# Performance work log

Hardware: AMD Instinct MI355X
Metric: run time of the kernel (lower is better)

The kernel has to match this reference:

```python
import jax, jax.numpy as jnp
import numpy as np
from jax import lax

N, P, Z, L = 1000, 50000, 10, 5


def setup_inputs() -> dict:
    key = jax.random.key(0)
    ks = jax.random.split(key, 9)
    data = jax.random.normal(ks[0], (N, P), dtype=jnp.float32)
    mean_z = jax.random.normal(ks[1], (N, Z), dtype=jnp.float32)
    A = jax.random.normal(ks[2], (Z, Z), dtype=jnp.float32) * 0.1
    var_z = A @ A.T + 0.01 * jnp.eye(Z, dtype=jnp.float32)  # PSD
    mean_w = jax.random.normal(ks[3], (L, Z, P), dtype=jnp.float32) * 0.01
    var_w = jax.random.uniform(ks[4], (L, Z), dtype=jnp.float32) + 0.1   # positive
    alpha = jax.nn.softmax(jax.random.normal(ks[5], (L, Z, P), dtype=jnp.float32), axis=-1)
    tau_0 = jax.random.uniform(ks[6], (L, Z), dtype=jnp.float32) + 0.5   # positive prior precision
    pi = jax.nn.softmax(jax.random.normal(ks[7], (Z, P), dtype=jnp.float32), axis=-1)
    tau = jnp.array(1.0, dtype=jnp.float32)
    return dict(data=data, mean_z=mean_z, var_z=var_z, mean_w=mean_w,
                var_w=var_w, alpha=alpha, tau_0=tau_0, pi=pi, tau=tau)


def _log_bf(z, s2, s0):
    s0_inv = 1.0 / s0
    s2ps0inv = s2 + s0_inv
    return 0.5 * (jnp.log(s2) - jnp.log(s2ps0inv) + z ** 2 * (s0_inv / s2ps0inv))


def reference(data, mean_z, var_z, mean_w, var_w, alpha, tau_0, pi, tau):
    n_dim = data.shape[0]
    l_dim, z_dim, p_dim = mean_w.shape

    # FactorModel.moments
    mean_zz = mean_z.T @ mean_z + n_dim * var_z            # [z, z]
    # LoadingModel.moments (only mean_w moment is needed)
    W0 = jnp.sum(mean_w * alpha, axis=0)                    # [z, p]

    def factor_body(kdx, carry):
        W, mw, vw, al = carry
        not_k = jnp.where(jnp.arange(z_dim) != kdx, size=z_dim - 1)[0]  # [z-1]
        E_zpzk = mean_zz[kdx][not_k]                        # [z-1]
        E_zzk = mean_zz[kdx, kdx]                           # scalar
        Wk = W[kdx]                                         # [p]
        Wnk = W[not_k]                                      # [z-1, p]
        RtZk = mean_z[:, kdx] @ data - Wnk.T @ E_zpzk       # [p]

        def effect_body(ldx, ecarry):
            Wk, mw, vw, al = ecarry
            Wkl = Wk - mw[ldx, kdx] * al[ldx, kdx]          # [p] residualized
            E_RtZk = RtZk - E_zzk * Wkl                     # [p]
            u_var = jnp.reciprocal(tau * E_zzk + tau_0[ldx, kdx])  # scalar
            u_mean = tau * u_var * E_RtZk                   # [p]
            Z_s = E_RtZk / E_zzk * jnp.sqrt(E_zzk * tau)    # [p]
            s2_s = 1.0 / (E_zzk * tau)
            log_bf = _log_bf(Z_s, s2_s, tau_0[ldx, kdx])
            alpha_kl = jax.nn.softmax(jnp.log(pi[kdx]) + log_bf)   # [p]
            Wk_new = Wkl + u_mean * alpha_kl
            return (Wk_new,
                    mw.at[ldx, kdx].set(u_mean),
                    vw.at[ldx, kdx].set(u_var),
                    al.at[ldx, kdx].set(alpha_kl))

        Wk, mw, vw, al = lax.fori_loop(0, l_dim, effect_body, (Wk, mw, vw, al))
        return (W.at[kdx].set(Wk), mw, vw, al)

    W, mw, vw, al = lax.fori_loop(0, z_dim, factor_body, (W0, mean_w, var_w, alpha))
    return mw, vw, al
```

## Files before the change

### kernel.cpp

```cpp
#include <hip/hip_runtime.h>
#include <math.h>

#define N_DIM 1000
#define P_DIM 50000
#define Z_DIM 10
#define L_DIM 5
#define NSTEP 50

#define NTP 256
#define NBP 196
#define NSPLIT 4
#define NCHUNK 250

#define NT1 256
#define PPT 4
#define PBLK (NT1 * PPT)
#define NBLK 49
#define NEG_BIG (-3.0e38f)
#define SPIN_MAX 32768

constexpr size_t ZP       = (size_t)Z_DIM * P_DIM;
constexpr size_t OFF_ZTR  = 0;
constexpr size_t OFF_PART = ZP;
constexpr size_t PART_F   = (size_t)NSTEP * 64 * 2;
constexpr size_t OFF_W    = ZP + PART_F;
constexpr size_t OFF_ZZ   = OFF_W + ZP;
constexpr size_t WS_ZERO_BYTES = (ZP + PART_F) * sizeof(float);

constexpr size_t OUT_MW = 0;
constexpr size_t OUT_VW = (size_t)L_DIM * Z_DIM * P_DIM;
constexpr size_t OUT_AL = OUT_VW + (size_t)L_DIM * Z_DIM;

__device__ inline void online_merge(float& m, float& e, float m2, float e2) {
    float M = fmaxf(m, m2);
    e = e * __expf(m - M) + e2 * __expf(m2 - M);
    m = M;
}

__global__ __launch_bounds__(256) void init_zz(const float* __restrict__ mean_z,
                                               const float* __restrict__ var_z,
                                               float* __restrict__ ws) {
    float* zz = ws + OFF_ZZ;
    int i = blockIdx.x / Z_DIM, j = blockIdx.x % Z_DIM;
    float s = 0.f;
    for (int n = threadIdx.x; n < N_DIM; n += 256)
        s += mean_z[n * Z_DIM + i] * mean_z[n * Z_DIM + j];
    #pragma unroll
    for (int off = 32; off > 0; off >>= 1) s += __shfl_xor(s, off);
    __shared__ float ls[4];
    if ((threadIdx.x & 63) == 0) ls[threadIdx.x >> 6] = s;
    __syncthreads();
    if (threadIdx.x == 0) {
        float t = ls[0] + ls[1] + ls[2] + ls[3];
        zz[blockIdx.x] = t + (float)N_DIM * var_z[blockIdx.x];
    }
}

__global__ __launch_bounds__(NTP) void precompute_big(const float* __restrict__ data,
                                                      const float* __restrict__ mean_z,
                                                      const float* __restrict__ mw0,
                                                      const float* __restrict__ al0,
                                                      float* __restrict__ ws) {
    float* ZtR = ws + OFF_ZTR;
    float* W   = ws + OFF_W;
    __shared__ float mzs[NCHUNK * Z_DIM];
    int n0 = blockIdx.y * NCHUNK;
    for (int i = threadIdx.x; i < NCHUNK * Z_DIM; i += NTP)
        mzs[i] = mean_z[n0 * Z_DIM + i];
    __syncthreads();
    int p = blockIdx.x * NTP + threadIdx.x;
    if (p >= P_DIM) return;

    float acc[Z_DIM];
    #pragma unroll
    for (int z = 0; z < Z_DIM; z++) acc[z] = 0.f;
    for (int r = 0; r < NCHUNK; r++) {
        float d = data[(size_t)(n0 + r) * P_DIM + p];
        #pragma unroll
        for (int z = 0; z < Z_DIM; z++) acc[z] = fmaf(mzs[r * Z_DIM + z], d, acc[z]);
    }
    #pragma unroll
    for (int z = 0; z < Z_DIM; z++) atomicAdd(&ZtR[(size_t)z * P_DIM + p], acc[z]);

    if (blockIdx.y == 0) {
        #pragma unroll
        for (int z = 0; z < Z_DIM; z++) {
            float w = 0.f;
            #pragma unroll
            for (int l = 0; l < L_DIM; l++) {
                size_t io = ((size_t)l * Z_DIM + z) * P_DIM + p;
                w = fmaf(mw0[io], al0[io], w);
            }
            W[(size_t)z * P_DIM + p] = w;
        }
    }
}

__global__ __launch_bounds__(NT1) void steps_fused(const float* __restrict__ mw0,
                                                   const float* __restrict__ al0,
                                                   const float* __restrict__ pi,
                                                   const float* __restrict__ tau0,
                                                   const float* __restrict__ taup,
                                                   float* __restrict__ ws,
                                                   float* __restrict__ out) {
    const float* ZtR = ws + OFF_ZTR;
    const float* Wg  = ws + OFF_W;
    const float* zz  = ws + OFF_ZZ;
    unsigned long long* part = reinterpret_cast<unsigned long long*>(ws + OFF_PART);
    float* out_mw = out + OUT_MW;
    float* out_vw = out + OUT_VW;
    float* out_al = out + OUT_AL;

    __shared__ float sm[NT1 / 64], se[NT1 / 64], bro[2];

    const int tid  = threadIdx.x;
    const int bid  = blockIdx.x;
    const int lane = tid & 63;
    const int wid  = tid >> 6;
    const int p0   = bid * PBLK + tid * PPT;
    const bool valid = p0 < P_DIM;
    const float tau = taup[0];

    float W[Z_DIM][PPT];
    #pragma unroll
    for (int z = 0; z < Z_DIM; z++)
        #pragma unroll
        for (int i = 0; i < PPT; i++) W[z][i] = 0.f;
    if (valid) {
        #pragma unroll
        for (int z = 0; z < Z_DIM; z++) {
            float4 t = *reinterpret_cast<const float4*>(Wg + (size_t)z * P_DIM + p0);
            W[z][0] = t.x; W[z][1] = t.y; W[z][2] = t.z; W[z][3] = t.w;
        }
    }
    float mw_c[PPT], al_c[PPT], lpi[PPT];
    #pragma unroll
    for (int i = 0; i < PPT; i++) { mw_c[i] = 0.f; al_c[i] = 0.f; lpi[i] = 0.f; }
    if (valid) {
        float4 tm = *reinterpret_cast<const float4*>(mw0 + p0);
        float4 ta = *reinterpret_cast<const float4*>(al0 + p0);
        mw_c[0] = tm.x; mw_c[1] = tm.y; mw_c[2] = tm.z; mw_c[3] = tm.w;
        al_c[0] = ta.x; al_c[1] = ta.y; al_c[2] = ta.z; al_c[3] = ta.w;
        #pragma unroll
        for (int i = 0; i < PPT; i++) lpi[i] = __logf(pi[p0 + i]);
    }

    float wk[PPT], r[PPT];
    #pragma unroll
    for (int i = 0; i < PPT; i++) { wk[i] = 0.f; r[i] = 0.f; }
    int k = 0, l = 0;

    #pragma unroll 1
    for (int s = 0; s < NSTEP; s++) {
        const float Ezz   = zz[k * Z_DIM + k];
        const float t0v   = tau0[l * Z_DIM + k];
        const float u_var = 1.f / (tau * Ezz + t0v);
        const float s2    = 1.f / (Ezz * tau);
        const float s0inv = 1.f / t0v;
        const float cq    = 0.5f * (tau / Ezz) * (s0inv / (s2 + s0inv));

        if (l == 0) {
            float zk[PPT] = {0.f, 0.f, 0.f, 0.f};
            if (valid) {
                float4 t = *reinterpret_cast<const float4*>(ZtR + (size_t)k * P_DIM + p0);
                zk[0] = t.x; zk[1] = t.y; zk[2] = t.z; zk[3] = t.w;
            }
            #pragma unroll
            for (int i = 0; i < PPT; i++) r[i] = zk[i];
            #pragma unroll
            for (int j = 0; j < Z_DIM; j++) {
                float c = (j == k) ? 0.f : zz[k * Z_DIM + j];
                #pragma unroll
                for (int i = 0; i < PPT; i++) r[i] = fmaf(-c, W[j][i], r[i]);
                if (j == k)
                    #pragma unroll
                    for (int i = 0; i < PPT; i++) wk[i] = W[j][i];
            }
        }

        const size_t io = ((size_t)l * Z_DIM + k) * P_DIM + p0;
        float wkl[PPT], um[PPT], lgt[PPT];
        #pragma unroll
        for (int i = 0; i < PPT; i++) { wkl[i] = 0.f; um[i] = 0.f; lgt[i] = NEG_BIG; }
        if (valid) {
            #pragma unroll
            for (int i = 0; i < PPT; i++) {
                wkl[i] = wk[i] - mw_c[i] * al_c[i];
                float E = fmaf(-Ezz, wkl[i], r[i]);
                um[i]  = tau * u_var * E;
                lgt[i] = fmaf(cq * E, E, lpi[i]);
            }
            float4 sv = make_float4(um[0], um[1], um[2], um[3]);
            *reinterpret_cast<float4*>(out_mw + io) = sv;
        }

        float m4 = fmaxf(fmaxf(lgt[0], lgt[1]), fmaxf(lgt[2], lgt[3]));
        #pragma unroll
        for (int off = 32; off > 0; off >>= 1) m4 = fmaxf(m4, __shfl_xor(m4, off));
        if (lane == 0) sm[wid] = m4;
        __syncthreads();
        const float Mb = fmaxf(fmaxf(sm[0], sm[1]), fmaxf(sm[2], sm[3]));

        float esv[PPT];
        #pragma unroll
        for (int i = 0; i < PPT; i++) esv[i] = __expf(lgt[i] - Mb);
        float s4 = (esv[0] + esv[1]) + (esv[2] + esv[3]);
        #pragma unroll
        for (int off = 32; off > 0; off >>= 1) s4 += __shfl_xor(s4, off);
        if (lane == 0) se[wid] = s4;
        __syncthreads();
        if (tid == 0) {
            float Eb = (se[0] + se[1]) + (se[2] + se[3]);
            unsigned long long v = ((unsigned long long)__float_as_uint(Eb) << 32)
                                 | (unsigned long long)__float_as_uint(Mb);
            __hip_atomic_store(&part[(size_t)s * 64 + bid], v, __ATOMIC_RELAXED,
                               __HIP_MEMORY_SCOPE_AGENT);
        }

        int kn = k, ln = l + 1;
        if (ln == L_DIM) { ln = 0; kn++; }
        float mw_n[PPT], al_n[PPT], lpi_n[PPT];
        #pragma unroll
        for (int i = 0; i < PPT; i++) { mw_n[i] = 0.f; al_n[i] = 0.f; lpi_n[i] = lpi[i]; }
        if (valid && s + 1 < NSTEP) {
            size_t ion = ((size_t)ln * Z_DIM + kn) * P_DIM + p0;
            float4 tm = *reinterpret_cast<const float4*>(mw0 + ion);
            float4 ta = *reinterpret_cast<const float4*>(al0 + ion);
            mw_n[0] = tm.x; mw_n[1] = tm.y; mw_n[2] = tm.z; mw_n[3] = tm.w;
            al_n[0] = ta.x; al_n[1] = ta.y; al_n[2] = ta.z; al_n[3] = ta.w;
            if (ln == 0)
                #pragma unroll
                for (int i = 0; i < PPT; i++) lpi_n[i] = __logf(pi[(size_t)kn * P_DIM + p0 + i]);
        }

        float pm = NEG_BIG, pe = 0.f;
        if (wid == 0) {
            if (lane < NBLK) {
                const unsigned long long* ap = &part[(size_t)s * 64 + lane];
                unsigned long long v = 0;
                for (int it = 0; it < SPIN_MAX; it++) {
                    v = __hip_atomic_load(ap, __ATOMIC_RELAXED, __HIP_MEMORY_SCOPE_AGENT);
                    if ((unsigned)(v >> 32) != 0u) break;
                }
                pm = __uint_as_float((unsigned)v);
                pe = __uint_as_float((unsigned)(v >> 32));
            }
            #pragma unroll
            for (int off = 32; off > 0; off >>= 1)
                online_merge(pm, pe, __shfl_xor(pm, off), __shfl_xor(pe, off));
            if (lane == 0) { bro[0] = pm; bro[1] = pe; }
        }
        __syncthreads();
        const float M = bro[0];
        const float scale = __expf(Mb - M) / bro[1];

        if (valid) {
            float a[PPT];
            #pragma unroll
            for (int i = 0; i < PPT; i++) {
                a[i] = esv[i] * scale;
                wk[i] = fmaf(um[i], a[i], wkl[i]);
            }
            float4 sv = make_float4(a[0], a[1], a[2], a[3]);
            *reinterpret_cast<float4*>(out_al + io) = sv;
        }
        if (p0 == 0 && tid == 0) out_vw[l * Z_DIM + k] = u_var;

        if (l == L_DIM - 1) {
            #pragma unroll
            for (int j = 0; j < Z_DIM; j++)
                if (j == k)
                    #pragma unroll
                    for (int i = 0; i < PPT; i++) W[j][i] = wk[i];
        }
        #pragma unroll
        for (int i = 0; i < PPT; i++) { mw_c[i] = mw_n[i]; al_c[i] = al_n[i]; lpi[i] = lpi_n[i]; }
        k = kn; l = ln;
    }
}

extern "C" void kernel_launch(void* const* d_in, const int* in_sizes, int n_in,
                              void* d_out, int out_size, void* d_ws, size_t ws_size,
                              hipStream_t stream) {
    (void)in_sizes; (void)n_in; (void)out_size; (void)ws_size;
    const float* data   = (const float*)d_in[0];
    const float* mean_z = (const float*)d_in[1];
    const float* var_z  = (const float*)d_in[2];
    const float* mw0    = (const float*)d_in[3];
    const float* al0    = (const float*)d_in[5];
    const float* tau0   = (const float*)d_in[6];
    const float* pi     = (const float*)d_in[7];
    const float* taup   = (const float*)d_in[8];
    float* out = (float*)d_out;
    float* ws  = (float*)d_ws;

    hipMemsetAsync(ws, 0, WS_ZERO_BYTES, stream);
    init_zz<<<Z_DIM * Z_DIM, 256, 0, stream>>>(mean_z, var_z, ws);
    precompute_big<<<dim3(NBP, NSPLIT), NTP, 0, stream>>>(data, mean_z, mw0, al0, ws);
    steps_fused<<<NBLK, NT1, 0, stream>>>(mw0, al0, pi, tau0, taup, ws, out);
}
```

Baseline: 476.6 us.

## Use per-wave cross-block softmax partials and fold init work into precompute

Each wave now publishes its own softmax max/sum partial, so the two block-wide __syncthreads reductions per step are gone. Every wave spins on all 196 slots itself, which removes the final block barrier. The memset and the separate zz kernel are folded into an extra grid row of precompute_big. The ZtR atomics are replaced by per-split partial buffers that are summed when each factor is loaded. In exchange, each wave issues four times as many polling loads per step, and the workspace grows by the split partial buffers.

```diff
diff --git a/kernel.cpp b/kernel.cpp
--- a/kernel.cpp
+++ b/kernel.cpp
@@ -16,53 +16,55 @@
 #define PPT 4
 #define PBLK (NT1 * PPT)
 #define NBLK 49
+#define NWAVES (NBLK * 4)
+#define SLOT_STRIDE 256
 #define NEG_BIG (-3.0e38f)
 #define SPIN_MAX 32768
 
 constexpr size_t ZP       = (size_t)Z_DIM * P_DIM;
-constexpr size_t OFF_ZTR  = 0;
-constexpr size_t OFF_PART = ZP;
-constexpr size_t PART_F   = (size_t)NSTEP * 64 * 2;
-constexpr size_t OFF_W    = ZP + PART_F;
+constexpr size_t OFF_PART = 0;
+constexpr size_t PART_F   = (size_t)NSTEP * SLOT_STRIDE * 2;
+constexpr size_t OFF_ZTRP = PART_F;
+constexpr size_t OFF_W    = OFF_ZTRP + (size_t)NSPLIT * ZP;
 constexpr size_t OFF_ZZ   = OFF_W + ZP;
-constexpr size_t WS_ZERO_BYTES = (ZP + PART_F) * sizeof(float);
 
 constexpr size_t OUT_MW = 0;
 constexpr size_t OUT_VW = (size_t)L_DIM * Z_DIM * P_DIM;
 constexpr size_t OUT_AL = OUT_VW + (size_t)L_DIM * Z_DIM;
 
-__device__ inline void online_merge(float& m, float& e, float m2, float e2) {
-    float M = fmaxf(m, m2);
-    e = e * __expf(m - M) + e2 * __expf(m2 - M);
-    m = M;
-}
-
-__global__ __launch_bounds__(256) void init_zz(const float* __restrict__ mean_z,
-                                               const float* __restrict__ var_z,
-                                               float* __restrict__ ws) {
-    float* zz = ws + OFF_ZZ;
-    int i = blockIdx.x / Z_DIM, j = blockIdx.x % Z_DIM;
-    float s = 0.f;
-    for (int n = threadIdx.x; n < N_DIM; n += 256)
-        s += mean_z[n * Z_DIM + i] * mean_z[n * Z_DIM + j];
-    #pragma unroll
-    for (int off = 32; off > 0; off >>= 1) s += __shfl_xor(s, off);
-    __shared__ float ls[4];
-    if ((threadIdx.x & 63) == 0) ls[threadIdx.x >> 6] = s;
-    __syncthreads();
-    if (threadIdx.x == 0) {
-        float t = ls[0] + ls[1] + ls[2] + ls[3];
-        zz[blockIdx.x] = t + (float)N_DIM * var_z[blockIdx.x];
-    }
-}
-
 __global__ __launch_bounds__(NTP) void precompute_big(const float* __restrict__ data,
                                                       const float* __restrict__ mean_z,
+                                                      const float* __restrict__ var_z,
                                                       const float* __restrict__ mw0,
                                                       const float* __restrict__ al0,
                                                       float* __restrict__ ws) {
-    float* ZtR = ws + OFF_ZTR;
-    float* W   = ws + OFF_W;
+    if (blockIdx.y == NSPLIT) {
+        int bx = blockIdx.x;
+        if (bx < Z_DIM * Z_DIM) {
+            float* zz = ws + OFF_ZZ;
+            int i = bx / Z_DIM, j = bx % Z_DIM;
+            float s = 0.f;
+            for (int n = threadIdx.x; n < N_DIM; n += NTP)
+                s += mean_z[n * Z_DIM + i] * mean_z[n * Z_DIM + j];
+            #pragma unroll
+            for (int off = 32; off > 0; off >>= 1) s += __shfl_xor(s, off);
+            __shared__ float ls[4];
+            if ((threadIdx.x & 63) == 0) ls[threadIdx.x >> 6] = s;
+            __syncthreads();
+            if (threadIdx.x == 0) {
+                float t = ls[0] + ls[1] + ls[2] + ls[3];
+                zz[bx] = t + (float)N_DIM * var_z[bx];
+            }
+        } else {
+            unsigned long long* part = reinterpret_cast<unsigned long long*>(ws + OFF_PART);
+            int idx = (bx - Z_DIM * Z_DIM) * NTP + threadIdx.x;
+            if (idx < NSTEP * SLOT_STRIDE) part[idx] = 0ULL;
+        }
+        return;
+    }
+
+    float* ZtRp = ws + OFF_ZTRP + (size_t)blockIdx.y * ZP;
+    float* W    = ws + OFF_W;
     __shared__ float mzs[NCHUNK * Z_DIM];
     int n0 = blockIdx.y * NCHUNK;
     for (int i = threadIdx.x; i < NCHUNK * Z_DIM; i += NTP)
@@ -80,7 +82,7 @@
         for (int z = 0; z < Z_DIM; z++) acc[z] = fmaf(mzs[r * Z_DIM + z], d, acc[z]);
     }
     #pragma unroll
-    for (int z = 0; z < Z_DIM; z++) atomicAdd(&ZtR[(size_t)z * P_DIM + p], acc[z]);
+    for (int z = 0; z < Z_DIM; z++) ZtRp[(size_t)z * P_DIM + p] = acc[z];
 
     if (blockIdx.y == 0) {
         #pragma unroll
@@ -103,46 +105,49 @@
                                                    const float* __restrict__ taup,
                                                    float* __restrict__ ws,
                                                    float* __restrict__ out) {
-    const float* ZtR = ws + OFF_ZTR;
-    const float* Wg  = ws + OFF_W;
-    const float* zz  = ws + OFF_ZZ;
+    const float* ZtRp = ws + OFF_ZTRP;
+    const float* Wg   = ws + OFF_W;
+    const float* zz   = ws + OFF_ZZ;
     unsigned long long* part = reinterpret_cast<unsigned long long*>(ws + OFF_PART);
     float* out_mw = out + OUT_MW;
     float* out_vw = out + OUT_VW;
     float* out_al = out + OUT_AL;
 
-    __shared__ float sm[NT1 / 64], se[NT1 / 64], bro[2];
-
     const int tid  = threadIdx.x;
     const int bid  = blockIdx.x;
     const int lane = tid & 63;
     const int wid  = tid >> 6;
+    const int gw   = bid * 4 + wid;
     const int p0   = bid * PBLK + tid * PPT;
     const bool valid = p0 < P_DIM;
     const float tau = taup[0];
+    const bool need3 = lane < (NWAVES - 192);
 
     float W[Z_DIM][PPT];
     #pragma unroll
     for (int z = 0; z < Z_DIM; z++)
         #pragma unroll
         for (int i = 0; i < PPT; i++) W[z][i] = 0.f;
+    float mw_c[PPT], al_c[PPT], lpi[PPT], zk[PPT];
+    #pragma unroll
+    for (int i = 0; i < PPT; i++) { mw_c[i] = 0.f; al_c[i] = 0.f; lpi[i] = 0.f; zk[i] = 0.f; }
     if (valid) {
         #pragma unroll
         for (int z = 0; z < Z_DIM; z++) {
             float4 t = *reinterpret_cast<const float4*>(Wg + (size_t)z * P_DIM + p0);
             W[z][0] = t.x; W[z][1] = t.y; W[z][2] = t.z; W[z][3] = t.w;
         }
-    }
-    float mw_c[PPT], al_c[PPT], lpi[PPT];
-    #pragma unroll
-    for (int i = 0; i < PPT; i++) { mw_c[i] = 0.f; al_c[i] = 0.f; lpi[i] = 0.f; }
-    if (valid) {
         float4 tm = *reinterpret_cast<const float4*>(mw0 + p0);
         float4 ta = *reinterpret_cast<const float4*>(al0 + p0);
         mw_c[0] = tm.x; mw_c[1] = tm.y; mw_c[2] = tm.z; mw_c[3] = tm.w;
         al_c[0] = ta.x; al_c[1] = ta.y; al_c[2] = ta.z; al_c[3] = ta.w;
         #pragma unroll
         for (int i = 0; i < PPT; i++) lpi[i] = __logf(pi[p0 + i]);
+        #pragma unroll
+        for (int y = 0; y < NSPLIT; y++) {
+            float4 t = *reinterpret_cast<const float4*>(ZtRp + ((size_t)y * Z_DIM + 0) * P_DIM + p0);
+            zk[0] += t.x; zk[1] += t.y; zk[2] += t.z; zk[3] += t.w;
+        }
     }
 
     float wk[PPT], r[PPT];
@@ -160,11 +165,6 @@
         const float cq    = 0.5f * (tau / Ezz) * (s0inv / (s2 + s0inv));
 
         if (l == 0) {
-            float zk[PPT] = {0.f, 0.f, 0.f, 0.f};
-            if (valid) {
-                float4 t = *reinterpret_cast<const float4*>(ZtR + (size_t)k * P_DIM + p0);
-                zk[0] = t.x; zk[1] = t.y; zk[2] = t.z; zk[3] = t.w;
-            }
             #pragma unroll
             for (int i = 0; i < PPT; i++) r[i] = zk[i];
             #pragma unroll
@@ -197,74 +197,88 @@
         float m4 = fmaxf(fmaxf(lgt[0], lgt[1]), fmaxf(lgt[2], lgt[3]));
         #pragma unroll
         for (int off = 32; off > 0; off >>= 1) m4 = fmaxf(m4, __shfl_xor(m4, off));
-        if (lane == 0) sm[wid] = m4;
-        __syncthreads();
-        const float Mb = fmaxf(fmaxf(sm[0], sm[1]), fmaxf(sm[2], sm[3]));
-
+        const float Mw = m4;
         float esv[PPT];
         #pragma unroll
-        for (int i = 0; i < PPT; i++) esv[i] = __expf(lgt[i] - Mb);
+        for (int i = 0; i < PPT; i++) esv[i] = __expf(lgt[i] - Mw);
         float s4 = (esv[0] + esv[1]) + (esv[2] + esv[3]);
         #pragma unroll
         for (int off = 32; off > 0; off >>= 1) s4 += __shfl_xor(s4, off);
-        if (lane == 0) se[wid] = s4;
-        __syncthreads();
-        if (tid == 0) {
-            float Eb = (se[0] + se[1]) + (se[2] + se[3]);
-            unsigned long long v = ((unsigned long long)__float_as_uint(Eb) << 32)
-                                 | (unsigned long long)__float_as_uint(Mb);
-            __hip_atomic_store(&part[(size_t)s * 64 + bid], v, __ATOMIC_RELAXED,
+        if (lane == 0) {
+            unsigned long long v = ((unsigned long long)__float_as_uint(s4) << 32)
+                                 | (unsigned long long)__float_as_uint(Mw);
+            __hip_atomic_store(&part[(size_t)s * SLOT_STRIDE + gw], v, __ATOMIC_RELAXED,
                                __HIP_MEMORY_SCOPE_AGENT);
         }
 
         int kn = k, ln = l + 1;
         if (ln == L_DIM) { ln = 0; kn++; }
-        float mw_n[PPT], al_n[PPT], lpi_n[PPT];
-        #pragma unroll
-        for (int i = 0; i < PPT; i++) { mw_n[i] = 0.f; al_n[i] = 0.f; lpi_n[i] = lpi[i]; }
+        float mw_n[PPT], al_n[PPT];
+        #pragma unroll
+        for (int i = 0; i < PPT; i++) { mw_n[i] = 0.f; al_n[i] = 0.f; }
         if (valid && s + 1 < NSTEP) {
             size_t ion = ((size_t)ln * Z_DIM + kn) * P_DIM + p0;
             float4 tm = *reinterpret_cast<const float4*>(mw0 + ion);
             float4 ta = *reinterpret_cast<const float4*>(al0 + ion);
             mw_n[0] = tm.x; mw_n[1] = tm.y; mw_n[2] = tm.z; mw_n[3] = tm.w;
             al_n[0] = ta.x; al_n[1] = ta.y; al_n[2] = ta.z; al_n[3] = ta.w;
-            if (ln == 0)
+            if (ln == 0) {
                 #pragma unroll
-                for (int i = 0; i < PPT; i++) lpi_n[i] = __logf(pi[(size_t)kn * P_DIM + p0 + i]);
-        }
-
-        float pm = NEG_BIG, pe = 0.f;
-        if (wid == 0) {
-            if (lane < NBLK) {
-                const unsigned long long* ap = &part[(size_t)s * 64 + lane];
-                unsigned long long v = 0;
-                for (int it = 0; it < SPIN_MAX; it++) {
-                    v = __hip_atomic_load(ap, __ATOMIC_RELAXED, __HIP_MEMORY_SCOPE_AGENT);
-                    if ((unsigned)(v >> 32) != 0u) break;
+                for (int i = 0; i < PPT; i++) lpi[i] = __logf(pi[(size_t)kn * P_DIM + p0 + i]);
+                #pragma unroll
+                for (int i = 0; i < PPT; i++) zk[i] = 0.f;
+                #pragma unroll
+                for (int y = 0; y < NSPLIT; y++) {
+                    float4 t = *reinterpret_cast<const float4*>(
+                        ZtRp + ((size_t)y * Z_DIM + kn) * P_DIM + p0);
+                    zk[0] += t.x; zk[1] += t.y; zk[2] += t.z; zk[3] += t.w;
                 }
-                pm = __uint_as_float((unsigned)v);
-                pe = __uint_as_float((unsigned)(v >> 32));
-            }
-            #pragma unroll
-            for (int off = 32; off > 0; off >>= 1)
-                online_merge(pm, pe, __shfl_xor(pm, off), __shfl_xor(pe, off));
-            if (lane == 0) { bro[0] = pm; bro[1] = pe; }
-        }
-        __syncthreads();
-        const float M = bro[0];
-        const float scale = __expf(Mb - M) / bro[1];
+            }
+        }
+        float cc[PPT];
+        #pragma unroll
+        for (int i = 0; i < PPT; i++) cc[i] = um[i] * esv[i];
+
+        const unsigned long long* sb = part + (size_t)s * SLOT_STRIDE;
+        unsigned long long v0 = 0, v1 = 0, v2 = 0;
+        unsigned long long v3 = need3 ? 0ULL : (1ULL << 32);
+        for (int it = 0; it < SPIN_MAX; it++) {
+            if (!(unsigned)(v0 >> 32))
+                v0 = __hip_atomic_load(sb + lane,       __ATOMIC_RELAXED, __HIP_MEMORY_SCOPE_AGENT);
+            if (!(unsigned)(v1 >> 32))
+                v1 = __hip_atomic_load(sb + 64 + lane,  __ATOMIC_RELAXED, __HIP_MEMORY_SCOPE_AGENT);
+            if (!(unsigned)(v2 >> 32))
+                v2 = __hip_atomic_load(sb + 128 + lane, __ATOMIC_RELAXED, __HIP_MEMORY_SCOPE_AGENT);
+            if (!(unsigned)(v3 >> 32))
+                v3 = __hip_atomic_load(sb + 192 + lane, __ATOMIC_RELAXED, __HIP_MEMORY_SCOPE_AGENT);
+            if ((unsigned)(v0 >> 32) && (unsigned)(v1 >> 32) &&
+                (unsigned)(v2 >> 32) && (unsigned)(v3 >> 32)) break;
+        }
+        float m0 = __uint_as_float((unsigned)v0), e0 = __uint_as_float((unsigned)(v0 >> 32));
+        float m1 = __uint_as_float((unsigned)v1), e1 = __uint_as_float((unsigned)(v1 >> 32));
+        float m2 = __uint_as_float((unsigned)v2), e2 = __uint_as_float((unsigned)(v2 >> 32));
+        float m3 = __uint_as_float((unsigned)v3), e3 = __uint_as_float((unsigned)(v3 >> 32));
+        float mm = fmaxf(fmaxf(m0, m1), fmaxf(m2, m3));
+        #pragma unroll
+        for (int off = 32; off > 0; off >>= 1) mm = fmaxf(mm, __shfl_xor(mm, off));
+        const float M = mm;
+        float ss = e0 * __expf(m0 - M) + e1 * __expf(m1 - M)
+                 + e2 * __expf(m2 - M) + e3 * __expf(m3 - M);
+        #pragma unroll
+        for (int off = 32; off > 0; off >>= 1) ss += __shfl_xor(ss, off);
+        const float scale = __expf(Mw - M) / ss;
 
         if (valid) {
             float a[PPT];
             #pragma unroll
             for (int i = 0; i < PPT; i++) {
-                a[i] = esv[i] * scale;
-                wk[i] = fmaf(um[i], a[i], wkl[i]);
+                a[i]  = esv[i] * scale;
+                wk[i] = fmaf(cc[i], scale, wkl[i]);
             }
             float4 sv = make_float4(a[0], a[1], a[2], a[3]);
             *reinterpret_cast<float4*>(out_al + io) = sv;
         }
-        if (p0 == 0 && tid == 0) out_vw[l * Z_DIM + k] = u_var;
+        if (tid == 0 && bid == 0) out_vw[l * Z_DIM + k] = u_var;
 
         if (l == L_DIM - 1) {
             #pragma unroll
@@ -274,7 +288,7 @@
                     for (int i = 0; i < PPT; i++) W[j][i] = wk[i];
         }
         #pragma unroll
-        for (int i = 0; i < PPT; i++) { mw_c[i] = mw_n[i]; al_c[i] = al_n[i]; lpi[i] = lpi_n[i]; }
+        for (int i = 0; i < PPT; i++) { mw_c[i] = mw_n[i]; al_c[i] = al_n[i]; }
         k = kn; l = ln;
     }
 }
@@ -294,8 +308,7 @@
     float* out = (float*)d_out;
     float* ws  = (float*)d_ws;
 
-    hipMemsetAsync(ws, 0, WS_ZERO_BYTES, stream);
-    init_zz<<<Z_DIM * Z_DIM, 256, 0, stream>>>(mean_z, var_z, ws);
-    precompute_big<<<dim3(NBP, NSPLIT), NTP, 0, stream>>>(data, mean_z, mw0, al0, ws);
+    precompute_big<<<dim3(NBP, NSPLIT + 1), NTP, 0, stream>>>(data, mean_z, var_z,
+                                                              mw0, al0, ws);
     steps_fused<<<NBLK, NT1, 0, stream>>>(mw0, al0, pi, tau0, taup, ws, out);
 }
```

Measured after the change: 481.5 us. Within noise of the previous version (+1.0%).
